# Kernel optimization log

Hardware: AMD Instinct MI355X
Metric: run time of the kernel (lower is better)

The kernel has to match this reference:

```python
import jax, jax.numpy as jnp
import numpy as np

LN_EPS = 1e-5


def _layernorm(h, gamma, beta):
    mu = jnp.mean(h, axis=-1, keepdims=True)
    var = jnp.var(h, axis=-1, keepdims=True)
    return (h - mu) * jax.lax.rsqrt(var + LN_EPS) * gamma + beta


def _simple_attention(q, k, v):
    # DIFFormer 'simple' kernel, num_heads=1: global-Frobenius-normalized q,k,
    # linear attention numerator + uniform component, denominator + N.
    n = q.shape[0]
    qs = q / jnp.linalg.norm(q)            # [N, M]
    ks = k / jnp.linalg.norm(k)            # [N, M]
    kvs = jnp.einsum('lm,ld->md', ks, v)   # [M, D]
    num = jnp.einsum('nm,md->nd', qs, kvs) + jnp.sum(v, axis=0)  # [N, D]
    den = jnp.einsum('nm,m->n', qs, jnp.sum(ks, axis=0)) + jnp.asarray(n, q.dtype)
    return num / den[:, None]


def reference(x, edge_index, W1, b1, Wq, bq, Wk, bk, gamma, beta, alpha, Wr, br, wgt):
    n = x.shape[0]
    row, col = edge_index[0], edge_index[1]
    # symmetric GCN normalization (degree of destination index, as in DIFFormer)
    deg = jax.ops.segment_sum(jnp.ones_like(col, dtype=x.dtype), col, num_segments=n)
    inv_sqrt = jnp.where(deg > 0, 1.0 / jnp.sqrt(deg), 0.0)
    w_edge = inv_sqrt[col] * inv_sqrt[row]  # [E]

    def gcn_conv(v):
        # out[i] = sum_{e: col[e]==i} w[e] * v[row[e]]
        return jax.ops.segment_sum(w_edge[:, None] * v[row], col, num_segments=n)

    def conv(h):
        q = h @ Wq + bq
        k = h @ Wk + bk
        v = h                              # use_weight=False -> value = source input
        return _simple_attention(q, k, v) + gcn_conv(v)

    R = jax.nn.relu(x @ W1 + b1)           # [N, H]
    Ts = [R]
    for _ in range(3):                      # three calls of the SAME shared conv
        Rn = conv(R)
        R = alpha * Rn + (1.0 - alpha) * R  # residual blend
        R = _layernorm(R, gamma, beta)      # shared LayerNorm
        Ts.append(R)

    # multi-head linear readout + learned weighted sum (dropout = identity in eval)
    res = jnp.stack([Ts[i] @ Wr[i] + br[i] for i in range(4)], axis=0)  # [4, N]
    out = jnp.einsum('i,in->n', wgt, res)[:, None]                       # [N, 1]
    return out


def setup_inputs():
    key = jax.random.key(0)
    ks = jax.random.split(key, 8)
    N, E, F_IN, H = 100000, 3200000, 58, 256
    x = jax.random.normal(ks[0], (N, F_IN), dtype=jnp.float32)
    edge_index = jax.random.randint(ks[1], (2, E), 0, N, dtype=jnp.int32)
    s_in = 1.0 / np.sqrt(F_IN)
    s_h = 1.0 / np.sqrt(H)
    return {
        'x': x,
        'edge_index': edge_index,
        'W1': jax.random.normal(ks[2], (F_IN, H), dtype=jnp.float32) * s_in,
        'b1': jnp.zeros((H,), jnp.float32),
        'Wq': jax.random.normal(ks[3], (H, H), dtype=jnp.float32) * s_h,
        'bq': jnp.zeros((H,), jnp.float32),
        'Wk': jax.random.normal(ks[4], (H, H), dtype=jnp.float32) * s_h,
        'bk': jnp.zeros((H,), jnp.float32),
        'gamma': jnp.ones((H,), jnp.float32),
        'beta': jnp.zeros((H,), jnp.float32),
        'alpha': jnp.float32(0.5),
        'Wr': jax.random.normal(ks[5], (4, H), dtype=jnp.float32) * s_h,
        'br': jnp.zeros((4,), jnp.float32),
        'wgt': jnp.array([0.5, 0.5, 0.5, 0.5], jnp.float32),
    }
```

## Files before the change

kernel.cpp:

```cpp
#include <hip/hip_runtime.h>

#define H 256
#define FIN 58
#define LN_EPS 1e-5f
#define EPB 8192
#define SBW 11

typedef __bf16 bf16x8 __attribute__((ext_vector_type(8)));
typedef float f32x16 __attribute__((ext_vector_type(16)));
typedef float f32x2 __attribute__((ext_vector_type(2)));

union FragU {
  ushort u[8];
  bf16x8 v;
};


__device__ __forceinline__ float wave_sum(float v) {
#pragma unroll
  for (int off = 1; off < 64; off <<= 1) v += __shfl_xor(v, off, 64);
  return v;
}

__device__ __forceinline__ float half_sum(float v) {
#pragma unroll
  for (int off = 1; off < 32; off <<= 1) v += __shfl_xor(v, off, 64);
  return v;
}

__device__ __forceinline__ float block_sum(float v, volatile float* red) {
  const int tid = threadIdx.x;
  v = wave_sum(v);
  __syncthreads();
  if ((tid & 63) == 0) red[tid >> 6] = v;
  __syncthreads();
  return red[0] + red[1] + red[2] + red[3];
}

__device__ __forceinline__ ushort f2bf(float f) {
  unsigned u = __float_as_uint(f);
  unsigned r = (u + 0x7FFFu + ((u >> 16) & 1u)) >> 16;
  return (ushort)r;
}

__device__ __forceinline__ float bf2f(ushort u) {
  return __uint_as_float((unsigned)u << 16);
}

#if __has_builtin(__builtin_amdgcn_cvt_pk_fp8_f32) && __has_builtin(__builtin_amdgcn_cvt_pk_f32_fp8)
__device__ __forceinline__ unsigned pack_fp8x4(float a, float b, float c, float d) {
  int v = 0;
  v = __builtin_amdgcn_cvt_pk_fp8_f32(a, b, v, false);
  v = __builtin_amdgcn_cvt_pk_fp8_f32(c, d, v, true);
  return (unsigned)v;
}
__device__ __forceinline__ void unpack_fp8x2_acc(f32x2& lo, f32x2& hi, unsigned v) {
  lo += __builtin_amdgcn_cvt_pk_f32_fp8((int)v, false);
  hi += __builtin_amdgcn_cvt_pk_f32_fp8((int)v, true);
}
#else
__device__ __forceinline__ unsigned char f2e4m3_1(float f) {
  unsigned u = __float_as_uint(f);
  unsigned s = (u >> 31) << 7;
  float a = fabsf(f);
  if (a >= 448.0f) return (unsigned char)(s | 0x7E);
  if (a < 0.0009765625f) return (unsigned char)s;
  int e;
  float m = frexpf(a, &e);
  int E = e - 1 + 7;
  if (E >= 1) {
    int mm = (int)rintf((m * 2.0f - 1.0f) * 8.0f);
    if (mm == 8) { mm = 0; E++; }
    return (unsigned char)(s | (E << 3) | mm);
  }
  int mm = (int)rintf(a * 512.0f);
  if (mm > 7) return (unsigned char)(s | (1 << 3));
  return (unsigned char)(s | mm);
}
__device__ __forceinline__ unsigned pack_fp8x4(float a, float b, float c, float d) {
  return (unsigned)f2e4m3_1(a) | ((unsigned)f2e4m3_1(b) << 8) |
         ((unsigned)f2e4m3_1(c) << 16) | ((unsigned)f2e4m3_1(d) << 24);
}
__device__ __forceinline__ float e4m3f_1(unsigned v) {
  int s = (v >> 7) & 1, E = (v >> 3) & 15, m = v & 7;
  float mag = E ? ldexpf(1.0f + m * 0.125f, E - 7) : ldexpf((float)m, -9);
  return s ? -mag : mag;
}
__device__ __forceinline__ void unpack_fp8x2_acc(f32x2& lo, f32x2& hi, unsigned v) {
  lo[0] += e4m3f_1(v & 255);
  lo[1] += e4m3f_1((v >> 8) & 255);
  hi[0] += e4m3f_1((v >> 16) & 255);
  hi[1] += e4m3f_1(v >> 24);
}
#endif


__global__ __launch_bounds__(512) void k_b1(const int* __restrict__ row,
                                            const int* __restrict__ col,
                                            unsigned* __restrict__ breg,
                                            int* __restrict__ gcnt,
                                            int cap2, int E, int nsb) {
  __shared__ unsigned stage[EPB];
  __shared__ int lh[65], lbase[65], lcur[64], gclaim[64];
  const int tid = threadIdx.x;
  const int e0 = blockIdx.x * EPB;
  const int cnt = min(EPB, E - e0);
  if (tid < 64) lh[tid] = 0;
  __syncthreads();
  for (int i = tid; i < cnt; i += 512) atomicAdd(&lh[col[e0 + i] >> SBW], 1);
  __syncthreads();
  if (tid == 0) {
    int acc = 0;
    for (int b = 0; b < nsb; b++) { lbase[b] = acc; acc += lh[b]; }
    lbase[nsb] = acc;
  }
  __syncthreads();
  if (tid < nsb) {
    gclaim[tid] = atomicAdd(&gcnt[tid], lh[tid]);
    lcur[tid] = lbase[tid];
  }
  __syncthreads();
  for (int i = tid; i < cnt; i += 512) {
    int c = col[e0 + i];
    int b = c >> SBW;
    int s = atomicAdd(&lcur[b], 1);
    stage[s] = ((unsigned)row[e0 + i] << SBW) | (unsigned)(c & ((1 << SBW) - 1));
  }
  __syncthreads();
  for (int i = tid; i < cnt; i += 512) {
    int lo = 0, hi = nsb;
    while (hi - lo > 1) {
      int mid = (lo + hi) >> 1;
      if (lbase[mid] <= i) lo = mid; else hi = mid;
    }
    int off = gclaim[lo] + (i - lbase[lo]);
    if (off < cap2) breg[(size_t)lo * cap2 + off] = stage[i];
  }
}

__global__ __launch_bounds__(512) void k_degB2(const unsigned* __restrict__ breg,
                                               const int* __restrict__ gcnt, int cap2,
                                               int* __restrict__ deg,
                                               float* __restrict__ invs, int N) {
  __shared__ int lcnt[1 << SBW];
  const int b = blockIdx.x, tid = threadIdx.x, base = b << SBW;
  for (int i = tid; i < (1 << SBW); i += 512) lcnt[i] = 0;
  __syncthreads();
  const int cnt = min(gcnt[b], cap2);
  const unsigned* p = breg + (size_t)b * cap2;
  for (int i = tid; i < cnt; i += 512) atomicAdd(&lcnt[p[i] & ((1 << SBW) - 1)], 1);
  __syncthreads();
  for (int i = tid; i < (1 << SBW); i += 512) {
    int d = base + i;
    if (d < N) {
      int c = lcnt[i];
      deg[d] = c;
      invs[d] = (c > 0) ? (1.0f / sqrtf((float)c)) : 0.0f;
    }
  }
}

__global__ __launch_bounds__(512) void k_b2(const unsigned* __restrict__ breg,
                                            const int* __restrict__ gcnt, int cap2,
                                            int* __restrict__ offs16,
                                            const int* __restrict__ bsum,
                                            int* __restrict__ eb, int N) {
  __shared__ int loffs[1 << SBW];
  __shared__ int lcur[1 << SBW];
  const int b = blockIdx.x, tid = threadIdx.x, base = b << SBW;
  for (int i = tid; i < (1 << SBW); i += 512) {
    int d = base + i;
    if (d < N) {
      int o = offs16[d] + bsum[d >> 10];
      loffs[i] = o;
      offs16[d] = o;
    } else {
      loffs[i] = 0;
    }
    lcur[i] = 0;
  }
  __syncthreads();
  const int cnt = min(gcnt[b], cap2);
  const unsigned* p = breg + (size_t)b * cap2;
  for (int i = tid; i < cnt; i += 512) {
    unsigned rc = p[i];
    int lc = rc & ((1 << SBW) - 1);
    int slot = atomicAdd(&lcur[lc], 1);
    eb[loffs[lc] + slot] = (int)(rc >> SBW);
  }
  __syncthreads();
  for (int i = tid; i < (1 << SBW); i += 512) {
    int d = base + i;
    if (d < N) {
      int c = lcur[i];
      int pad = (c + 15) & ~15;
      int o = loffs[i];
      for (int j = c; j < pad; j++) eb[o + j] = N;
    }
  }
}

__global__ __launch_bounds__(1024) void k_scan1(const int* __restrict__ deg,
                                                int* __restrict__ offs16,
                                                int* __restrict__ bsum, int N) {
  __shared__ int buf[1024];
  const int tid = threadIdx.x;
  const int gid = blockIdx.x * 1024 + tid;
  int v = (gid < N) ? ((deg[gid] + 15) & ~15) : 0;
  buf[tid] = v;
  __syncthreads();
  for (int off = 1; off < 1024; off <<= 1) {
    int x = (tid >= off) ? buf[tid - off] : 0;
    __syncthreads();
    buf[tid] += x;
    __syncthreads();
  }
  if (gid < N) offs16[gid] = buf[tid] - v;
  if (tid == 1023) bsum[blockIdx.x] = buf[1023];
}

__global__ __launch_bounds__(1024) void k_scan2(int* __restrict__ bsum, int nb) {
  __shared__ int buf[1024];
  const int tid = threadIdx.x;
  int v = (tid < nb) ? bsum[tid] : 0;
  buf[tid] = v;
  __syncthreads();
  for (int off = 1; off < 1024; off <<= 1) {
    int x = (tid >= off) ? buf[tid - off] : 0;
    __syncthreads();
    buf[tid] += x;
    __syncthreads();
  }
  if (tid < nb) bsum[tid] = buf[tid] - v;
}

__global__ void k_prep(const float* __restrict__ Wq, const float* __restrict__ Wk,
                       const float* __restrict__ bq, const float* __restrict__ bk,
                       float* __restrict__ P, float* __restrict__ Q, float* __restrict__ K2,
                       float* __restrict__ pb, float* __restrict__ qb,
                       float* __restrict__ wb, float* __restrict__ kb,
                       float* __restrict__ sconst) {
  __shared__ float red[4];
  const int b = blockIdx.x, tid = threadIdx.x;
  if (b < 768) {
    const int f = b & 255, which = b >> 8;
    const float* A = (which == 2) ? Wk : Wq;
    const float* Bm = (which == 1) ? Wq : Wk;
    float acc = 0.0f;
    for (int m = 0; m < H; m++) acc = fmaf(A[f * H + m], Bm[tid * H + m], acc);
    float* D = (which == 0) ? P : ((which == 1) ? Q : K2);
    D[f * H + tid] = acc;
  } else {
    float a1 = 0, a2 = 0, a3 = 0, a4 = 0;
    for (int m = 0; m < H; m++) {
      float wqv = Wq[tid * H + m], wkv = Wk[tid * H + m];
      a1 = fmaf(wqv, bk[m], a1);
      a2 = fmaf(wqv, bq[m], a2);
      a3 = fmaf(wkv, bq[m], a3);
      a4 = fmaf(wkv, bk[m], a4);
    }
    pb[tid] = a1; qb[tid] = a2; wb[tid] = a3; kb[tid] = a4;
    float c0 = block_sum(bq[tid] * bk[tid], red);
    float c1 = block_sum(bq[tid] * bq[tid], red);
    float c2 = block_sum(bk[tid] * bk[tid], red);
    if (tid == 0) { sconst[0] = c0; sconst[1] = c1; sconst[2] = c2; }
  }
}

__global__ void k_fc1(const float* __restrict__ x, const float* __restrict__ W1,
                      const float* __restrict__ b1, const float* __restrict__ Wr,
                      const float* __restrict__ br, const float* __restrict__ wgt,
                      ushort* __restrict__ R0, float* __restrict__ out, int N) {
  __shared__ __align__(16) float lx[16 * FIN];
  __shared__ float red2[4][16];
  const int tid = threadIdx.x;
  const int n0 = blockIdx.x * 16;
  for (int idx = tid; idx < 16 * FIN / 4; idx += 256)
    ((float4*)lx)[idx] = ((const float4*)(x + (size_t)n0 * FIN))[idx];
  __syncthreads();
  float acc[16];
  const float bias = b1[tid];
#pragma unroll
  for (int r = 0; r < 16; r++) acc[r] = bias;
  for (int f = 0; f < FIN; f++) {
    float wv = W1[f * H + tid];
#pragma unroll
    for (int r = 0; r < 16; r++) acc[r] = fmaf(lx[r * FIN + f], wv, acc[r]);
  }
  const float wr0 = Wr[tid];
#pragma unroll
  for (int r = 0; r < 16; r++) {
    acc[r] = fmaxf(acc[r], 0.0f);
    int n = n0 + r;
    if (n < N) R0[(size_t)n * H + tid] = f2bf(acc[r]);
  }
#pragma unroll
  for (int r = 0; r < 16; r++) {
    float s = wave_sum(acc[r] * wr0);
    if ((tid & 63) == 0) red2[tid >> 6][r] = s;
  }
  __syncthreads();
  if (tid < 16) {
    int n = n0 + tid;
    if (n < N)
      out[n] = wgt[0] * (red2[0][tid] + red2[1][tid] + red2[2][tid] + red2[3][tid] + br[0]);
  }
}

__global__ __launch_bounds__(512, 2) void k_Gm(const ushort* __restrict__ Rb,
                                               const float* __restrict__ invs,
                                               ushort* __restrict__ Gslab,
                                               unsigned* __restrict__ Rf8,
                                               float* __restrict__ csl, int N) {
  __shared__ ushort sbT[2][256 * 32];
  const int tid = threadIdx.x;
  const int lane = tid & 63;
  const int wid = tid >> 6;
  const int wrow = (wid & 1) * 128;
  const int wcol = (wid >> 1) * 64;
  const int l31 = lane & 31;
  const int lhi = lane >> 5;

  const int TC = (N + 31) >> 5;
  const int cbase = TC >> 8;
  const int crem = TC & 255;
  const int b = blockIdx.x;
  const int startc = b * cbase + min(b, crem);
  const int nch = cbase + (b < crem ? 1 : 0);
  const int rowbase = startc * 32;

  const int rp = tid >> 5;
  const int fg = tid & 31;
  const int k2 = rp * 2;

  f32x16 acc[4][2];
#pragma unroll
  for (int s = 0; s < 4; s++)
#pragma unroll
    for (int t = 0; t < 2; t++)
#pragma unroll
      for (int e = 0; e < 16; e++) acc[s][t][e] = 0.0f;

  float cs[8];
#pragma unroll
  for (int i = 0; i < 8; i++) cs[i] = 0.0f;

  int4 la, lb;
  float sc0, sc1;

  auto load_chunk = [&](int ch) {
    int g0 = rowbase + ch * 32 + k2;
    const int4* s0 = (const int4*)(Rb + (size_t)g0 * H + fg * 8);
    const int4* s1 = (const int4*)(Rb + (size_t)(g0 + 1) * H + fg * 8);
    la = (g0 < N) ? s0[0] : make_int4(0, 0, 0, 0);
    lb = (g0 + 1 < N) ? s1[0] : make_int4(0, 0, 0, 0);
    sc0 = (g0 < N) ? invs[g0] : 0.0f;
    sc1 = (g0 + 1 < N) ? invs[g0 + 1] : 0.0f;
  };

  auto write_chunk = [&](int ch, int buf) {
    int g0 = rowbase + ch * 32 + k2;
    const ushort* pa = (const ushort*)&la;
    const ushort* pbu = (const ushort*)&lb;
    const int blk = (k2 & 24) ^ ((fg & 3) << 3);
    uint* dst = (uint*)sbT[buf];
#pragma unroll
    for (int i = 0; i < 8; i++) {
      float av = bf2f(pa[i]), bv = bf2f(pbu[i]);
      cs[i] += av + bv;
      unsigned val = (unsigned)pa[i] | ((unsigned)pbu[i] << 16);
      int f = fg * 8 + i;
      dst[f * 16 + ((blk + (k2 & 7)) >> 1)] = val;
    }
    if (g0 < N) {
      unsigned w0 = pack_fp8x4(bf2f(pa[0]) * sc0, bf2f(pa[1]) * sc0,
                               bf2f(pa[2]) * sc0, bf2f(pa[3]) * sc0);
      unsigned w1 = pack_fp8x4(bf2f(pa[4]) * sc0, bf2f(pa[5]) * sc0,
                               bf2f(pa[6]) * sc0, bf2f(pa[7]) * sc0);
      *(uint2*)&Rf8[(size_t)g0 * 64 + fg * 2] = make_uint2(w0, w1);
    }
    if (g0 + 1 < N) {
      unsigned w0 = pack_fp8x4(bf2f(pbu[0]) * sc1, bf2f(pbu[1]) * sc1,
                               bf2f(pbu[2]) * sc1, bf2f(pbu[3]) * sc1);
      unsigned w1 = pack_fp8x4(bf2f(pbu[4]) * sc1, bf2f(pbu[5]) * sc1,
                               bf2f(pbu[6]) * sc1, bf2f(pbu[7]) * sc1);
      *(uint2*)&Rf8[(size_t)(g0 + 1) * 64 + fg * 2] = make_uint2(w0, w1);
    }
  };

  auto compute = [&](int buf) {
    const ushort* bp = sbT[buf];
#pragma unroll
    for (int ks = 0; ks < 2; ks++) {
      const int kb = ks * 16 + lhi * 8;
      FragU fr[6];
#pragma unroll
      for (int s = 0; s < 6; s++) {
        const int cb = (s < 4) ? (wrow + 32 * s + l31) : (wcol + 32 * (s - 4) + l31);
        const int off = cb * 32 + (kb ^ (((cb >> 3) & 3) << 3));
        *(int4*)fr[s].u = *(const int4*)(bp + off);
      }
#pragma unroll
      for (int s = 0; s < 4; s++)
#pragma unroll
        for (int t = 0; t < 2; t++)
          acc[s][t] = __builtin_amdgcn_mfma_f32_32x32x16_bf16(fr[s].v, fr[4 + t].v,
                                                              acc[s][t], 0, 0, 0);
    }
  };

  load_chunk(0);
  write_chunk(0, 0);
  __syncthreads();
  int cur = 0;
  for (int c = 0; c < nch; c++) {
    if (c + 1 < nch) load_chunk(c + 1);
    compute(cur);
    if (c + 1 < nch) write_chunk(c + 1, cur ^ 1);
    __syncthreads();
    cur ^= 1;
  }

  ushort* Gs = Gslab + (size_t)b * 65536;
#pragma unroll
  for (int s = 0; s < 4; s++)
#pragma unroll
    for (int t = 0; t < 2; t++) {
      const int n0c = wcol + 32 * t + l31;
#pragma unroll
      for (int r = 0; r < 16; r++) {
        const int row = wrow + 32 * s + (r & 3) + 8 * (r >> 2) + 4 * lhi;
        Gs[row * 256 + n0c] = f2bf(acc[s][t][r]);
      }
    }

  __syncthreads();
  float* fl = (float*)sbT;
#pragma unroll
  for (int i = 0; i < 8; i++) fl[rp * 256 + fg * 8 + i] = cs[i];
  __syncthreads();
  if (tid < 256) {
    float v = 0.0f;
    for (int j = 0; j < 16; j++) v += fl[j * 256 + tid];
    csl[(size_t)b * 256 + tid] = v;
  }
}

__global__ void k_Gr(const ushort* __restrict__ Gslab, const float* __restrict__ csl,
                     const float* __restrict__ Q, const float* __restrict__ K2,
                     float* __restrict__ G, float* __restrict__ vsum,
                     float2* __restrict__ spart, int nslab) {
  __shared__ float red[4];
  const int b = blockIdx.x, t = threadIdx.x;
  const int i = b * 256 + t;
  float s0 = 0, s1 = 0, s2 = 0, s3 = 0;
  int j = 0;
  for (; j + 3 < nslab; j += 4) {
    s0 += bf2f(Gslab[(size_t)j * 65536 + i]);
    s1 += bf2f(Gslab[(size_t)(j + 1) * 65536 + i]);
    s2 += bf2f(Gslab[(size_t)(j + 2) * 65536 + i]);
    s3 += bf2f(Gslab[(size_t)(j + 3) * 65536 + i]);
  }
  float s = s0 + s1 + s2 + s3;
  for (; j < nslab; j++) s += bf2f(Gslab[(size_t)j * 65536 + i]);
  G[i] = s;
  float dq = block_sum(s * Q[i], red);
  float dk = block_sum(s * K2[i], red);
  if (t == 0) spart[b] = make_float2(dq, dk);
  float v = 0.0f;
  for (int u = t; u < nslab; u += 256) v += csl[(size_t)u * 256 + b];
  v = block_sum(v, red);
  if (t == 0) vsum[b] = v;
}

__global__ void k_small(const float* __restrict__ G, const float* __restrict__ vsum,
                        const float* __restrict__ P, const float* __restrict__ pb,
                        const float* __restrict__ wb, const float* __restrict__ sconst,
                        const float* __restrict__ qb, const float* __restrict__ kbv,
                        const float2* __restrict__ spart,
                        ushort* __restrict__ Mt, float* __restrict__ cvec,
                        float* __restrict__ dvec, float* __restrict__ scal, int N) {
  __shared__ float red[4];
  const int b = blockIdx.x, tid = threadIdx.x;
  if (b < 256) {
    float acc = 0.0f;
    for (int m = 0; m < H; m++) acc = fmaf(P[b * H + m], G[m * H + tid], acc);
    Mt[(size_t)tid * H + b] = f2bf(acc + pb[b] * vsum[tid]);
  } else if (b == 256) {
    float acc = 0.0f;
    for (int f = 0; f < H; f++) acc = fmaf(wb[f], G[f * H + tid], acc);
    cvec[tid] = acc + sconst[0] * vsum[tid];
  } else if (b == 257) {
    float acc = 0.0f;
    for (int m = 0; m < H; m++) acc = fmaf(P[tid * H + m], vsum[m], acc);
    dvec[tid] = acc + (float)N * pb[tid];
  } else {
    float2 sp = spart[tid];
    float dq = block_sum(sp.x, red);
    float dk = block_sum(sp.y, red);
    float s1 = block_sum(qb[tid] * vsum[tid], red);
    float s2 = block_sum(kbv[tid] * vsum[tid], red);
    float s3 = block_sum(wb[tid] * vsum[tid], red);
    if (tid == 0) {
      float sq = dq + 2.0f * s1 + (float)N * sconst[1];
      float sk = dk + 2.0f * s2 + (float)N * sconst[2];
      scal[2] = 1.0f / (sqrtf(sq) * sqrtf(sk));
      scal[3] = s3 + (float)N * sconst[0];
    }
  }
}

__global__ __launch_bounds__(512) void k_N(const ushort* __restrict__ Rb,
                                           const ushort* __restrict__ Mt,
                                           ushort* __restrict__ numb, int N) {
  const int tid = threadIdx.x;
  const int lane = tid & 63;
  const int wid = tid >> 6;
  const int l31 = lane & 31;
  const int lhi = lane >> 5;
  const int wrow = (wid & 3) * 32;
  const int wcol = (wid >> 2) * 128;
  const int rowbase = blockIdx.x * 128;

  f32x16 acc[4];
#pragma unroll
  for (int t = 0; t < 4; t++)
#pragma unroll
    for (int e = 0; e < 16; e++) acc[t][e] = 0.0f;

  const ushort* aptr = Rb + (size_t)(rowbase + wrow + l31) * H;

  for (int kc = 0; kc < 16; kc++) {
    const int kb = kc * 16 + lhi * 8;
    FragU fa;
    *(int4*)fa.u = *(const int4*)(aptr + kb);
    FragU fb0, fb1, fb2, fb3;
    *(int4*)fb0.u = *(const int4*)(Mt + (size_t)(wcol + 0 + l31) * H + kb);
    *(int4*)fb1.u = *(const int4*)(Mt + (size_t)(wcol + 32 + l31) * H + kb);
    *(int4*)fb2.u = *(const int4*)(Mt + (size_t)(wcol + 64 + l31) * H + kb);
    *(int4*)fb3.u = *(const int4*)(Mt + (size_t)(wcol + 96 + l31) * H + kb);
    acc[0] = __builtin_amdgcn_mfma_f32_32x32x16_bf16(fa.v, fb0.v, acc[0], 0, 0, 0);
    acc[1] = __builtin_amdgcn_mfma_f32_32x32x16_bf16(fa.v, fb1.v, acc[1], 0, 0, 0);
    acc[2] = __builtin_amdgcn_mfma_f32_32x32x16_bf16(fa.v, fb2.v, acc[2], 0, 0, 0);
    acc[3] = __builtin_amdgcn_mfma_f32_32x32x16_bf16(fa.v, fb3.v, acc[3], 0, 0, 0);
  }

#pragma unroll
  for (int t = 0; t < 4; t++) {
    const int col = wcol + 32 * t + l31;
#pragma unroll
    for (int r = 0; r < 16; r++) {
      const int row = rowbase + wrow + (r & 3) + 8 * (r >> 2) + 4 * lhi;
      if (row < N) numb[(size_t)row * H + col] = f2bf(acc[t][r]);
    }
  }
}

__global__ __launch_bounds__(256) void k_C(
    const ushort* __restrict__ Rb, ushort* __restrict__ Rnext,
    const ushort* __restrict__ numb, const unsigned* __restrict__ Rf8,
    const int* __restrict__ eb, const float* __restrict__ invs,
    const float* __restrict__ cvec, const float* __restrict__ dvec,
    const float* __restrict__ vsum, const float* __restrict__ scal,
    const int* __restrict__ offs16, const int* __restrict__ deg,
    const float* __restrict__ alphap, const float* __restrict__ gamma,
    const float* __restrict__ beta, const float* __restrict__ Wr,
    const float* __restrict__ br, const float* __restrict__ wgt,
    float* __restrict__ out, int N, int layer, int last) {
  const int tid = threadIdx.x, lane = tid & 63, wv = tid >> 6;
  const int half = lane >> 5, hl = lane & 31;
  const int d0 = hl * 8;
  const int n0 = blockIdx.x * 32 + wv * 8;

  const float invn = scal[2], denc = scal[3];
  const float al = alphap[0], om = 1.0f - al;
  const float4 dvA = *(const float4*)&dvec[d0];
  const float4 dvB = *(const float4*)&dvec[d0 + 4];
  const float4 cvA = *(const float4*)&cvec[d0];
  const float4 cvB = *(const float4*)&cvec[d0 + 4];
  const float4 vsA = *(const float4*)&vsum[d0];
  const float4 vsB = *(const float4*)&vsum[d0 + 4];
  const float4 gmA = *(const float4*)&gamma[d0];
  const float4 gmB = *(const float4*)&gamma[d0 + 4];
  const float4 btA = *(const float4*)&beta[d0];
  const float4 btB = *(const float4*)&beta[d0 + 4];
  const float4 wrA = *(const float4*)&Wr[layer * H + d0];
  const float4 wrB = *(const float4*)&Wr[layer * H + d0 + 4];
  const float wl = wgt[layer], bl = br[layer];

  for (int r = 0; r < 4; r++) {
    const int n = n0 + r * 2 + half;
    const bool valid = n < N;
    const int ns = valid ? n : 0;

    const int4 rv = *(const int4*)&Rb[(size_t)ns * H + d0];
    const int4 nv = *(const int4*)&numb[(size_t)ns * H + d0];
    const ushort* rp = (const ushort*)&rv;
    const ushort* np = (const ushort*)&nv;
    float old[8], num[8];
#pragma unroll
    for (int j = 0; j < 8; j++) { old[j] = bf2f(rp[j]); num[j] = bf2f(np[j]); }

    float p = old[0] * dvA.x + old[1] * dvA.y + old[2] * dvA.z + old[3] * dvA.w +
              old[4] * dvB.x + old[5] * dvB.y + old[6] * dvB.z + old[7] * dvB.w;
    p = half_sum(p);
    const float rden = 1.0f / ((p + denc) * invn + (float)N);

    f32x2 a01 = {0.f, 0.f}, a23 = {0.f, 0.f}, a45 = {0.f, 0.f}, a67 = {0.f, 0.f};
    const int st = offs16[ns];
    const int nbch = valid ? ((deg[ns] + 15) >> 4) : 0;
    const int4* pe = (const int4*)(eb + st);
    const int woff = hl * 2;
    for (int b = 0; b < nbch; b++, pe += 4) {
      int4 q0 = pe[0], q1 = pe[1], q2 = pe[2], q3 = pe[3];
      const int srcs[16] = {q0.x, q0.y, q0.z, q0.w, q1.x, q1.y, q1.z, q1.w,
                            q2.x, q2.y, q2.z, q2.w, q3.x, q3.y, q3.z, q3.w};
      uint2 g[16];
#pragma unroll
      for (int i = 0; i < 16; i++)
        g[i] = *(const uint2*)&Rf8[((size_t)srcs[i] << 6) + woff];
#pragma unroll
      for (int i = 0; i < 16; i++) {
        unpack_fp8x2_acc(a01, a23, g[i].x);
        unpack_fp8x2_acc(a45, a67, g[i].y);
      }
    }
    const float sn = invs[ns];
    float ag[8] = {a01[0] * sn, a01[1] * sn, a23[0] * sn, a23[1] * sn,
                   a45[0] * sn, a45[1] * sn, a67[0] * sn, a67[1] * sn};

    const float cva[8] = {cvA.x, cvA.y, cvA.z, cvA.w, cvB.x, cvB.y, cvB.z, cvB.w};
    const float vsa[8] = {vsA.x, vsA.y, vsA.z, vsA.w, vsB.x, vsB.y, vsB.z, vsB.w};
    float hv[8];
#pragma unroll
    for (int j = 0; j < 8; j++)
      hv[j] = al * (((num[j] + cva[j]) * invn + vsa[j]) * rden + ag[j]) + om * old[j];

    float s = 0.0f, s2 = 0.0f;
#pragma unroll
    for (int j = 0; j < 8; j++) { s += hv[j]; s2 += hv[j] * hv[j]; }
    s = half_sum(s);
    s2 = half_sum(s2);
    const float mu = s * (1.0f / H);
    const float var = s2 * (1.0f / H) - mu * mu;
    const float rs = rsqrtf(var + LN_EPS);

    const float gma[8] = {gmA.x, gmA.y, gmA.z, gmA.w, gmB.x, gmB.y, gmB.z, gmB.w};
    const float bta[8] = {btA.x, btA.y, btA.z, btA.w, btB.x, btB.y, btB.z, btB.w};
    const float wra[8] = {wrA.x, wrA.y, wrA.z, wrA.w, wrB.x, wrB.y, wrB.z, wrB.w};
    float y[8], rp2 = 0.0f;
    ushort yo[8];
#pragma unroll
    for (int j = 0; j < 8; j++) {
      y[j] = (hv[j] - mu) * rs * gma[j] + bta[j];
      yo[j] = f2bf(y[j]);
      rp2 += y[j] * wra[j];
    }
    if (!last && valid) *(int4*)&Rnext[(size_t)n * H + d0] = *(int4*)yo;
    rp2 = half_sum(rp2);
    if (hl == 0 && valid) out[n] += wl * (rp2 + bl);
  }
}


extern "C" void kernel_launch(void* const* d_in, const int* in_sizes, int n_in,
                              void* d_out, int out_size, void* d_ws, size_t ws_size,
                              hipStream_t stream) {
  const float* x = (const float*)d_in[0];
  const int* ei = (const int*)d_in[1];
  const float* W1 = (const float*)d_in[2];
  const float* b1 = (const float*)d_in[3];
  const float* Wq = (const float*)d_in[4];
  const float* bq = (const float*)d_in[5];
  const float* Wk = (const float*)d_in[6];
  const float* bk = (const float*)d_in[7];
  const float* gamma = (const float*)d_in[8];
  const float* beta = (const float*)d_in[9];
  const float* alphap = (const float*)d_in[10];
  const float* Wr = (const float*)d_in[11];
  const float* br = (const float*)d_in[12];
  const float* wgt = (const float*)d_in[13];
  float* out = (float*)d_out;

  const int N = in_sizes[0] / FIN;
  const int E = in_sizes[1] / 2;
  const int* row = ei;
  const int* col = ei + E;

  char* w = (char*)d_ws;
  auto alloc = [&](size_t bytes) -> char* {
    char* p = w;
    w += (bytes + 255) & ~(size_t)255;
    return p;
  };
  const size_t RB = (size_t)(N + 128) * H * sizeof(ushort);
  ushort* Rb0 = (ushort*)alloc(RB);
  ushort* Rb1 = (ushort*)alloc(RB);
  ushort* numb = (ushort*)alloc(RB);
  unsigned* Rf8 = (unsigned*)alloc((size_t)(N + 1) * 64 * sizeof(unsigned));
  ushort* Mt = (ushort*)alloc(H * H * sizeof(ushort));
  float* G = (float*)alloc(H * H * sizeof(float));
  float* vsum = (float*)alloc(1024);
  float* scal = (float*)alloc(256);
  float* cvec = (float*)alloc(1024);
  float* dvec = (float*)alloc(1024);
  float* P = (float*)alloc(H * H * sizeof(float));
  float* Q = (float*)alloc(H * H * sizeof(float));
  float* K2 = (float*)alloc(H * H * sizeof(float));
  float* pb = (float*)alloc(1024);
  float* qb = (float*)alloc(1024);
  float* wb = (float*)alloc(1024);
  float* kb = (float*)alloc(1024);
  float* sconst = (float*)alloc(256);
  int* deg = (int*)alloc((size_t)N * 4);
  float* invs = (float*)alloc((size_t)N * 4);
  int* offs16 = (int*)alloc((size_t)(N + 1) * 4);
  int* bsum = (int*)alloc(1024 * 4);
  int* gcnt = (int*)alloc(64 * 4);
  const int nbG = 256;
  float* csl = (float*)alloc((size_t)nbG * 256 * sizeof(float));
  float2* spart = (float2*)alloc(256 * sizeof(float2));
  size_t EPAD = (size_t)E + 16 * (size_t)N;
  EPAD = (EPAD + 3) & ~(size_t)3;
  int* eb = (int*)alloc(EPAD * sizeof(int));

  const int NSB = (N + (1 << SBW) - 1) >> SBW;
  int cap2 = (E / (NSB > 0 ? NSB : 1)) * 2 + 4096;
  cap2 = (cap2 + 3) & ~3;
  unsigned* breg = (unsigned*)Rb1;
  ushort* Gslab = (ushort*)numb;

  hipMemsetAsync(gcnt, 0, 64 * 4, stream);
  hipMemsetAsync(Rf8 + (size_t)N * 64, 0, 64 * sizeof(unsigned), stream);

  const int nblk = (N + 1023) / 1024;
  const int nbB1 = (E + EPB - 1) / EPB;
  k_b1<<<nbB1, 512, 0, stream>>>(row, col, breg, gcnt, cap2, E, NSB);
  k_degB2<<<NSB, 512, 0, stream>>>(breg, gcnt, cap2, deg, invs, N);
  k_scan1<<<nblk, 1024, 0, stream>>>(deg, offs16, bsum, N);
  k_scan2<<<1, 1024, 0, stream>>>(bsum, nblk);
  k_b2<<<NSB, 512, 0, stream>>>(breg, gcnt, cap2, offs16, bsum, eb, N);
  k_prep<<<769, 256, 0, stream>>>(Wq, Wk, bq, bk, P, Q, K2, pb, qb, wb, kb, sconst);
  const int gRows16 = (N + 15) / 16;
  k_fc1<<<gRows16, 256, 0, stream>>>(x, W1, b1, Wr, br, wgt, Rb0, out, N);

  const int nbN = (N + 127) / 128;
  const int gRows32 = (N + 31) / 32;
  ushort* Rc = Rb0;
  ushort* Rn = Rb1;
  for (int it = 1; it <= 3; ++it) {
    k_Gm<<<nbG, 512, 0, stream>>>(Rc, invs, Gslab, Rf8, csl, N);
    k_Gr<<<256, 256, 0, stream>>>(Gslab, csl, Q, K2, G, vsum, spart, nbG);
    k_small<<<259, 256, 0, stream>>>(G, vsum, P, pb, wb, sconst, qb, kb, spart,
                                     Mt, cvec, dvec, scal, N);
    k_N<<<nbN, 512, 0, stream>>>(Rc, Mt, numb, N);
    k_C<<<gRows32, 256, 0, stream>>>(Rc, Rn, numb, Rf8, eb, invs, cvec, dvec, vsum, scal,
                                     offs16, deg, alphap, gamma, beta, Wr, br, wgt, out,
                                     N, it, (it == 3) ? 1 : 0);
    ushort* t = Rc; Rc = Rn; Rn = t;
  }
}
```

Before: 1.106 ms.

## Fuse numerator GEMM into combine kernel via shared-memory tile

Removes the separate k_N MFMA kernel. Each k_C block now computes its own 32x256 numerator tile with bf16 MFMA and keeps it in fp32 shared memory, so the bf16 numb buffer is no longer written to and read back from global memory. It also drops one launch per layer and keeps the numerator in fp32 instead of rounding to bf16. The cost is 32KB of LDS per block, which may lower occupancy for the latency-bound edge-gather loop, plus a block-wide barrier before the gather starts. Gslab gets its own allocation because numb no longer exists to alias.

```diff
diff --git a/kernel.cpp b/kernel.cpp
--- a/kernel.cpp
+++ b/kernel.cpp
@@ -510,55 +510,9 @@
   }
 }
 
-__global__ __launch_bounds__(512) void k_N(const ushort* __restrict__ Rb,
-                                           const ushort* __restrict__ Mt,
-                                           ushort* __restrict__ numb, int N) {
-  const int tid = threadIdx.x;
-  const int lane = tid & 63;
-  const int wid = tid >> 6;
-  const int l31 = lane & 31;
-  const int lhi = lane >> 5;
-  const int wrow = (wid & 3) * 32;
-  const int wcol = (wid >> 2) * 128;
-  const int rowbase = blockIdx.x * 128;
-
-  f32x16 acc[4];
-#pragma unroll
-  for (int t = 0; t < 4; t++)
-#pragma unroll
-    for (int e = 0; e < 16; e++) acc[t][e] = 0.0f;
-
-  const ushort* aptr = Rb + (size_t)(rowbase + wrow + l31) * H;
-
-  for (int kc = 0; kc < 16; kc++) {
-    const int kb = kc * 16 + lhi * 8;
-    FragU fa;
-    *(int4*)fa.u = *(const int4*)(aptr + kb);
-    FragU fb0, fb1, fb2, fb3;
-    *(int4*)fb0.u = *(const int4*)(Mt + (size_t)(wcol + 0 + l31) * H + kb);
-    *(int4*)fb1.u = *(const int4*)(Mt + (size_t)(wcol + 32 + l31) * H + kb);
-    *(int4*)fb2.u = *(const int4*)(Mt + (size_t)(wcol + 64 + l31) * H + kb);
-    *(int4*)fb3.u = *(const int4*)(Mt + (size_t)(wcol + 96 + l31) * H + kb);
-    acc[0] = __builtin_amdgcn_mfma_f32_32x32x16_bf16(fa.v, fb0.v, acc[0], 0, 0, 0);
-    acc[1] = __builtin_amdgcn_mfma_f32_32x32x16_bf16(fa.v, fb1.v, acc[1], 0, 0, 0);
-    acc[2] = __builtin_amdgcn_mfma_f32_32x32x16_bf16(fa.v, fb2.v, acc[2], 0, 0, 0);
-    acc[3] = __builtin_amdgcn_mfma_f32_32x32x16_bf16(fa.v, fb3.v, acc[3], 0, 0, 0);
-  }
-
-#pragma unroll
-  for (int t = 0; t < 4; t++) {
-    const int col = wcol + 32 * t + l31;
-#pragma unroll
-    for (int r = 0; r < 16; r++) {
-      const int row = rowbase + wrow + (r & 3) + 8 * (r >> 2) + 4 * lhi;
-      if (row < N) numb[(size_t)row * H + col] = f2bf(acc[t][r]);
-    }
-  }
-}
-
 __global__ __launch_bounds__(256) void k_C(
     const ushort* __restrict__ Rb, ushort* __restrict__ Rnext,
-    const ushort* __restrict__ numb, const unsigned* __restrict__ Rf8,
+    const ushort* __restrict__ Mt, const unsigned* __restrict__ Rf8,
     const int* __restrict__ eb, const float* __restrict__ invs,
     const float* __restrict__ cvec, const float* __restrict__ dvec,
     const float* __restrict__ vsum, const float* __restrict__ scal,
@@ -567,10 +521,37 @@
     const float* __restrict__ beta, const float* __restrict__ Wr,
     const float* __restrict__ br, const float* __restrict__ wgt,
     float* __restrict__ out, int N, int layer, int last) {
+  __shared__ __align__(16) float lnum[32 * 256];
   const int tid = threadIdx.x, lane = tid & 63, wv = tid >> 6;
   const int half = lane >> 5, hl = lane & 31;
   const int d0 = hl * 8;
-  const int n0 = blockIdx.x * 32 + wv * 8;
+  const int nb0 = blockIdx.x * 32;
+
+  {
+    f32x16 a0, a1;
+#pragma unroll
+    for (int e = 0; e < 16; e++) { a0[e] = 0.0f; a1[e] = 0.0f; }
+    const int wcol = wv * 64;
+    const ushort* aptr = Rb + (size_t)(nb0 + hl) * H;
+    const ushort* bptr0 = Mt + (size_t)(wcol + hl) * H;
+    const ushort* bptr1 = Mt + (size_t)(wcol + 32 + hl) * H;
+    for (int kc = 0; kc < 16; kc++) {
+      const int kb = kc * 16 + half * 8;
+      FragU fa, fb0, fb1;
+      *(int4*)fa.u = *(const int4*)(aptr + kb);
+      *(int4*)fb0.u = *(const int4*)(bptr0 + kb);
+      *(int4*)fb1.u = *(const int4*)(bptr1 + kb);
+      a0 = __builtin_amdgcn_mfma_f32_32x32x16_bf16(fa.v, fb0.v, a0, 0, 0, 0);
+      a1 = __builtin_amdgcn_mfma_f32_32x32x16_bf16(fa.v, fb1.v, a1, 0, 0, 0);
+    }
+#pragma unroll
+    for (int r = 0; r < 16; r++) {
+      const int row = (r & 3) + 8 * (r >> 2) + 4 * half;
+      lnum[row * 256 + wcol + hl] = a0[r];
+      lnum[row * 256 + wcol + 32 + hl] = a1[r];
+    }
+  }
+  __syncthreads();
 
   const float invn = scal[2], denc = scal[3];
   const float al = alphap[0], om = 1.0f - al;
@@ -589,17 +570,19 @@
   const float wl = wgt[layer], bl = br[layer];
 
   for (int r = 0; r < 4; r++) {
-    const int n = n0 + r * 2 + half;
+    const int lr = wv * 8 + r * 2 + half;
+    const int n = nb0 + lr;
     const bool valid = n < N;
     const int ns = valid ? n : 0;
 
     const int4 rv = *(const int4*)&Rb[(size_t)ns * H + d0];
-    const int4 nv = *(const int4*)&numb[(size_t)ns * H + d0];
     const ushort* rp = (const ushort*)&rv;
-    const ushort* np = (const ushort*)&nv;
-    float old[8], num[8];
-#pragma unroll
-    for (int j = 0; j < 8; j++) { old[j] = bf2f(rp[j]); num[j] = bf2f(np[j]); }
+    const float4 nvA = *(const float4*)&lnum[lr * 256 + d0];
+    const float4 nvB = *(const float4*)&lnum[lr * 256 + d0 + 4];
+    float old[8];
+#pragma unroll
+    for (int j = 0; j < 8; j++) old[j] = bf2f(rp[j]);
+    const float num[8] = {nvA.x, nvA.y, nvA.z, nvA.w, nvB.x, nvB.y, nvB.z, nvB.w};
 
     float p = old[0] * dvA.x + old[1] * dvA.y + old[2] * dvA.z + old[3] * dvA.w +
               old[4] * dvB.x + old[5] * dvB.y + old[6] * dvB.z + old[7] * dvB.w;
@@ -696,7 +679,7 @@
   const size_t RB = (size_t)(N + 128) * H * sizeof(ushort);
   ushort* Rb0 = (ushort*)alloc(RB);
   ushort* Rb1 = (ushort*)alloc(RB);
-  ushort* numb = (ushort*)alloc(RB);
+  ushort* Gslab = (ushort*)alloc((size_t)256 * 65536 * sizeof(ushort));
   unsigned* Rf8 = (unsigned*)alloc((size_t)(N + 1) * 64 * sizeof(unsigned));
   ushort* Mt = (ushort*)alloc(H * H * sizeof(ushort));
   float* G = (float*)alloc(H * H * sizeof(float));
@@ -728,7 +711,6 @@
   int cap2 = (E / (NSB > 0 ? NSB : 1)) * 2 + 4096;
   cap2 = (cap2 + 3) & ~3;
   unsigned* breg = (unsigned*)Rb1;
-  ushort* Gslab = (ushort*)numb;
 
   hipMemsetAsync(gcnt, 0, 64 * 4, stream);
   hipMemsetAsync(Rf8 + (size_t)N * 64, 0, 64 * sizeof(unsigned), stream);
@@ -744,7 +726,6 @@
   const int gRows16 = (N + 15) / 16;
   k_fc1<<<gRows16, 256, 0, stream>>>(x, W1, b1, Wr, br, wgt, Rb0, out, N);
 
-  const int nbN = (N + 127) / 128;
   const int gRows32 = (N + 31) / 32;
   ushort* Rc = Rb0;
   ushort* Rn = Rb1;
@@ -753,8 +734,7 @@
     k_Gr<<<256, 256, 0, stream>>>(Gslab, csl, Q, K2, G, vsum, spart, nbG);
     k_small<<<259, 256, 0, stream>>>(G, vsum, P, pb, wb, sconst, qb, kb, spart,
                                      Mt, cvec, dvec, scal, N);
-    k_N<<<nbN, 512, 0, stream>>>(Rc, Mt, numb, N);
-    k_C<<<gRows32, 256, 0, stream>>>(Rc, Rn, numb, Rf8, eb, invs, cvec, dvec, vsum, scal,
+    k_C<<<gRows32, 256, 0, stream>>>(Rc, Rn, Mt, Rf8, eb, invs, cvec, dvec, vsum, scal,
                                      offs16, deg, alphap, gamma, beta, Wr, br, wgt, out,
                                      N, it, (it == 3) ? 1 : 0);
     ushort* t = Rc; Rc = Rn; Rn = t;
```

New measurement: 1.059 ms. -4.3%, faster.
